# Performance work log

Hardware: AMD Instinct MI355X
Metric: run time of the kernel (lower is better)

Reference implementation:

```python
import jax, jax.numpy as jnp
import numpy as np

N, E_RAND, IN, HID, OUT = 10000, 320000, 512, 256, 256
E = E_RAND + N  # random edges + self loops
TEMP, LAM, LAMBDA_LOSS, BN_EPS = 0.5, 1e-3, 1.0, 1e-5


def _normalize(x):
    # F.normalize: x / max(||x||, 1e-12)
    return x / jnp.maximum(jnp.linalg.norm(x, axis=-1, keepdims=True), 1e-12)


def setup_inputs() -> dict:
    key = jax.random.key(0)
    ks = jax.random.split(key, 12)
    feat = jax.random.normal(ks[0], (N, IN), jnp.float32)
    loops = jnp.arange(N)
    src = jnp.concatenate([jax.random.randint(ks[1], (E_RAND,), 0, N), loops])
    dst = jnp.concatenate([jax.random.randint(ks[2], (E_RAND,), 0, N), loops])
    def lin(k, i, o):
        return jax.random.normal(k, (i, o), jnp.float32) / np.sqrt(i).astype(np.float32)
    return {
        'feat': feat,
        'W1': lin(ks[3], IN, HID), 'b1': jnp.zeros((HID,), jnp.float32),
        'W2': lin(ks[4], HID, OUT), 'b2': jnp.zeros((OUT,), jnp.float32),
        'Wt1': lin(ks[5], IN, HID), 'bt1': jnp.zeros((HID,), jnp.float32),
        'gamma': jnp.ones((HID,), jnp.float32), 'beta': jnp.zeros((HID,), jnp.float32),
        'Wt2': lin(ks[6], HID, OUT), 'bt2': jnp.zeros((OUT,), jnp.float32),
        'Wp': lin(ks[7], HID, HID), 'bp': jnp.zeros((HID,), jnp.float32),
        'src': src, 'dst': dst,
    }


def reference(feat, W1, b1, W2, b2, Wt1, bt1, gamma, beta, Wt2, bt2, Wp, bp, src, dst):
    n = feat.shape[0]
    ones = jnp.ones(src.shape, feat.dtype)
    deg_out = jax.ops.segment_sum(ones, src, num_segments=n)
    deg_in = jax.ops.segment_sum(ones, dst, num_segments=n)
    # symmetric GCN norm per edge (self-loops included so degrees >= 1)
    norm_e = jax.lax.rsqrt(deg_out)[src] * jax.lax.rsqrt(deg_in)[dst]

    def gconv(x, W, b):
        xw = x @ W  # [n, d_out]
        agg = jax.ops.segment_sum(xw[src] * norm_e[:, None], dst, num_segments=n)
        return agg + b

    # GCN encoder (2 layers, no LN)
    h = jax.nn.relu(gconv(feat, W1, b1))
    h = gconv(h, W2, b2)

    # target MLP encoder: linear -> BN(train) -> relu -> linear
    t = feat @ Wt1 + bt1
    mu = t.mean(0)
    var = t.var(0)  # biased, as BatchNorm normalization
    t = (t - mu) * jax.lax.rsqrt(var + BN_EPS) * gamma + beta
    trans = jax.nn.relu(t) @ Wt2 + bt2

    z = _normalize(h)                    # [n, d]
    q = _normalize(trans @ Wp + bp)      # projector (num_MLP=1)

    # pos_score: per-edge sum(z[u]*q[v])/temp, mean over in-edges at v
    sim_e = jnp.einsum('ed,ed->e', z[src], q[dst]) / TEMP
    pos = jax.ops.segment_sum(sim_e, dst, num_segments=n) / deg_in

    # neg_score (neg_sample=0): dense NxN similarity row-sums
    neg_sim = jnp.exp(z @ z.T / TEMP).sum(1)           # per-node
    neg_sim2 = LAM * jnp.exp(z @ q.T / TEMP).sum(1)    # per-node
    m_e = jnp.log(neg_sim[dst] + neg_sim2[src])
    neg = jax.ops.segment_sum(m_e, dst, num_segments=n) / deg_in

    loss = jnp.mean(-pos + LAMBDA_LOSS * neg)
    return loss
```

## Files before the change

kernel.cpp:

```cpp
#include <hip/hip_runtime.h>
#include <stdint.h>


#define TEMP_INV 2.0f
#define LAMC 1.0e-3f
#define SSCALE 1.6986436f

typedef __attribute__((ext_vector_type(8))) __bf16 bf16x8;
typedef __attribute__((ext_vector_type(4))) float f32x4;

__device__ __forceinline__ unsigned short f2bf(float x) {
  union { float f; unsigned int u; } v; v.f = x;
  unsigned int r = v.u + 0x7FFFu + ((v.u >> 16) & 1u);
  return (unsigned short)(r >> 16);
}

__device__ __forceinline__ void g2lds16(const void* gc, void* l) {
  void* g = const_cast<void*>(gc);
  __builtin_amdgcn_global_load_lds(
      (__attribute__((address_space(1))) void*)g,
      (__attribute__((address_space(3))) void*)l, 16, 0, 0);
}

__global__ void k_deg(const int* __restrict__ src, const int* __restrict__ dst,
                      float* deg_out, float* deg_in, int E) {
  int i = blockIdx.x * blockDim.x + threadIdx.x;
  if (i < E) {
    atomicAdd(&deg_out[src[i]], 1.0f);
    atomicAdd(&deg_in[dst[i]], 1.0f);
  }
}

__global__ void k_rdeg(const float* __restrict__ deg_out, const float* __restrict__ deg_in,
                       float* rdo, float* rdi, float* idi, int N) {
  int i = blockIdx.x * blockDim.x + threadIdx.x;
  if (i < N) {
    float o = deg_out[i], d = deg_in[i];
    rdo[i] = rsqrtf(o);
    rdi[i] = rsqrtf(d);
    idi[i] = 1.0f / d;
  }
}

__global__ void k_scan(const float* __restrict__ deg, int* __restrict__ off, int N, int E) {
  __shared__ int sm[1024];
  int tid = threadIdx.x;
  int chunk = (N + 1023) / 1024;
  int b = tid * chunk;
  int sum = 0;
  for (int j = 0; j < chunk; j++) { int i = b + j; if (i < N) sum += (int)deg[i]; }
  sm[tid] = sum;
  __syncthreads();
  for (int s = 1; s < 1024; s <<= 1) {
    int v = (tid >= s) ? sm[tid - s] : 0;
    __syncthreads();
    sm[tid] += v;
    __syncthreads();
  }
  int run = (tid == 0) ? 0 : sm[tid - 1];
  for (int j = 0; j < chunk; j++) {
    int i = b + j;
    if (i < N) { off[i] = run; run += (int)deg[i]; }
  }
  if (tid == 0) off[N] = E;
}

__global__ void k_fill(const int* __restrict__ src, const int* __restrict__ dst,
                       const int* __restrict__ off, int* cur,
                       const float* __restrict__ rdo, const float* __restrict__ rdi,
                       int* adj, float* aw, int E) {
  int e = blockIdx.x * blockDim.x + threadIdx.x;
  if (e < E) {
    int u = src[e], v = dst[e];
    int slot = off[v] + atomicAdd(&cur[v], 1);
    adj[slot] = u;
    aw[slot] = rdo[u] * rdi[v];
  }
}

template <int K, bool BIAS>
__global__ __launch_bounds__(256, 2) void k_gemm(const float* A, const float* __restrict__ W,
                                                 const float* __restrict__ bias, float* C, int M) {
  __shared__ float At[32][68];
  __shared__ float Wl[32][256];
  int tid = threadIdx.x;
  int rg = tid >> 4, cg = tid & 15;
  int r0 = rg * 4, cb = cg * 4;
  int row0 = blockIdx.x * 64;
  float acc[4][16] = {};
  for (int k0 = 0; k0 < K; k0 += 32) {
    __syncthreads();
#pragma unroll
    for (int t = 0; t < 2; t++) {
      int lin = tid + 256 * t;
      int r = lin >> 3, k4 = (lin & 7) * 4;
      int ar = row0 + r; if (ar >= M) ar = M - 1;
      float4 a4 = *(const float4*)(A + (size_t)ar * K + k0 + k4);
      At[k4 + 0][r] = a4.x; At[k4 + 1][r] = a4.y;
      At[k4 + 2][r] = a4.z; At[k4 + 3][r] = a4.w;
    }
#pragma unroll
    for (int t = 0; t < 8; t++) {
      int lin = tid + 256 * t;
      int kk = lin >> 6, c4 = (lin & 63) * 4;
      *(float4*)&Wl[kk][c4] = *(const float4*)(W + (size_t)(k0 + kk) * 256 + c4);
    }
    __syncthreads();
#pragma unroll
    for (int k = 0; k < 32; k++) {
      float4 a4 = *(const float4*)&At[k][r0];
      float av[4] = {a4.x, a4.y, a4.z, a4.w};
#pragma unroll
      for (int t = 0; t < 4; t++) {
        float4 w4 = *(const float4*)&Wl[k][64 * t + cb];
#pragma unroll
        for (int i = 0; i < 4; i++) {
          acc[i][4 * t + 0] += av[i] * w4.x;
          acc[i][4 * t + 1] += av[i] * w4.y;
          acc[i][4 * t + 2] += av[i] * w4.z;
          acc[i][4 * t + 3] += av[i] * w4.w;
        }
      }
    }
  }
#pragma unroll
  for (int i = 0; i < 4; i++) {
    int r = row0 + r0 + i;
    if (r < M) {
      float* crow = C + (size_t)r * 256;
#pragma unroll
      for (int t = 0; t < 4; t++) {
        int c = 64 * t + cb;
        float4 v = {acc[i][4 * t], acc[i][4 * t + 1], acc[i][4 * t + 2], acc[i][4 * t + 3]};
        if constexpr (BIAS) {
          float4 b4 = *(const float4*)(bias + c);
          v.x += b4.x; v.y += b4.y; v.z += b4.z; v.w += b4.w;
        }
        *(float4*)(crow + c) = v;
      }
    }
  }
}

__global__ __launch_bounds__(256, 2) void k_gemm2(const float* __restrict__ A,
                                                  const float* __restrict__ W1f,
                                                  const float* __restrict__ W2f,
                                                  const float* __restrict__ b2f,
                                                  float* __restrict__ C1, float* __restrict__ C2,
                                                  int M) {
  __shared__ float At[32][68];
  __shared__ float Wl[2][32][256];
  int tid = threadIdx.x;
  int rg = tid >> 4, cg = tid & 15;
  int r0 = rg * 4, cb = cg * 4;
  int row0 = blockIdx.x * 64;
  float acc1[4][16] = {};
  float acc2[4][16] = {};
  for (int k0 = 0; k0 < 512; k0 += 32) {
    __syncthreads();
#pragma unroll
    for (int t = 0; t < 2; t++) {
      int lin = tid + 256 * t;
      int r = lin >> 3, k4 = (lin & 7) * 4;
      int ar = row0 + r; if (ar >= M) ar = M - 1;
      float4 a4 = *(const float4*)(A + (size_t)ar * 512 + k0 + k4);
      At[k4 + 0][r] = a4.x; At[k4 + 1][r] = a4.y;
      At[k4 + 2][r] = a4.z; At[k4 + 3][r] = a4.w;
    }
#pragma unroll
    for (int t = 0; t < 8; t++) {
      int lin = tid + 256 * t;
      int kk = lin >> 6, c4 = (lin & 63) * 4;
      *(float4*)&Wl[0][kk][c4] = *(const float4*)(W1f + (size_t)(k0 + kk) * 256 + c4);
      *(float4*)&Wl[1][kk][c4] = *(const float4*)(W2f + (size_t)(k0 + kk) * 256 + c4);
    }
    __syncthreads();
#pragma unroll
    for (int k = 0; k < 32; k++) {
      float4 a4 = *(const float4*)&At[k][r0];
      float av[4] = {a4.x, a4.y, a4.z, a4.w};
#pragma unroll
      for (int t = 0; t < 4; t++) {
        float4 w4 = *(const float4*)&Wl[0][k][64 * t + cb];
        float4 u4 = *(const float4*)&Wl[1][k][64 * t + cb];
#pragma unroll
        for (int i = 0; i < 4; i++) {
          acc1[i][4 * t + 0] += av[i] * w4.x; acc1[i][4 * t + 1] += av[i] * w4.y;
          acc1[i][4 * t + 2] += av[i] * w4.z; acc1[i][4 * t + 3] += av[i] * w4.w;
          acc2[i][4 * t + 0] += av[i] * u4.x; acc2[i][4 * t + 1] += av[i] * u4.y;
          acc2[i][4 * t + 2] += av[i] * u4.z; acc2[i][4 * t + 3] += av[i] * u4.w;
        }
      }
    }
  }
#pragma unroll
  for (int i = 0; i < 4; i++) {
    int r = row0 + r0 + i;
    if (r < M) {
#pragma unroll
      for (int t = 0; t < 4; t++) {
        int c = 64 * t + cb;
        float4 v1 = {acc1[i][4 * t], acc1[i][4 * t + 1], acc1[i][4 * t + 2], acc1[i][4 * t + 3]};
        float4 v2 = {acc2[i][4 * t], acc2[i][4 * t + 1], acc2[i][4 * t + 2], acc2[i][4 * t + 3]};
        float4 b4 = *(const float4*)(b2f + c);
        v2.x += b4.x; v2.y += b4.y; v2.z += b4.z; v2.w += b4.w;
        *(float4*)(C1 + (size_t)r * 256 + c) = v1;
        *(float4*)(C2 + (size_t)r * 256 + c) = v2;
      }
    }
  }
}

__global__ void k_bnstat(const float* __restrict__ T, float* s, float* ss, int M) {
  int c = threadIdx.x;
  int r0 = blockIdx.x * 64;
  float a = 0, b = 0;
  for (int r = r0; r < r0 + 64 && r < M; r++) {
    float v = T[(size_t)r * 256 + c];
    a += v; b += v * v;
  }
  atomicAdd(&s[c], a);
  atomicAdd(&ss[c], b);
}

__global__ void k_bnrelu(float* T, const float* __restrict__ s, const float* __restrict__ ss,
                         const float* __restrict__ g, const float* __restrict__ b, int M) {
  int r = blockIdx.x, c = threadIdx.x;
  float invM = 1.0f / (float)M;
  float mu = s[c] * invM;
  float var = ss[c] * invM - mu * mu;
  float w = rsqrtf(var + 1e-5f) * g[c];
  float v = T[(size_t)r * 256 + c];
  v = (v - mu) * w + b[c];
  T[(size_t)r * 256 + c] = fmaxf(v, 0.0f);
}

template <bool UNIT, bool RELU>
__global__ __launch_bounds__(256) void k_agg(const float* __restrict__ X, const int* __restrict__ off,
                                             const int* __restrict__ adj, const float* __restrict__ w,
                                             const float* __restrict__ bias, float* __restrict__ Y, int N) {
  int wv = threadIdx.x >> 6, ln = threadIdx.x & 63;
  int v = blockIdx.x * 4 + wv;
  if (v >= N) return;
  int s0 = off[v], s1 = off[v + 1];
  const float4* X4 = (const float4*)X;
  float4 acc = {0, 0, 0, 0};
  for (int s = s0; s < s1; s++) {
    int u = adj[s];
    float wt = UNIT ? 1.0f : w[s];
    float4 x = X4[(size_t)u * 64 + ln];
    acc.x += wt * x.x; acc.y += wt * x.y; acc.z += wt * x.z; acc.w += wt * x.w;
  }
  if constexpr (!UNIT) {
    float4 b = ((const float4*)bias)[ln];
    acc.x += b.x; acc.y += b.y; acc.z += b.z; acc.w += b.w;
  }
  if constexpr (RELU) {
    acc.x = fmaxf(acc.x, 0.f); acc.y = fmaxf(acc.y, 0.f);
    acc.z = fmaxf(acc.z, 0.f); acc.w = fmaxf(acc.w, 0.f);
  }
  ((float4*)Y)[(size_t)v * 64 + ln] = acc;
}

__global__ __launch_bounds__(256) void k_norm(float* X, unsigned short* Xb, int N, int NPAD) {
  int wv = threadIdx.x >> 6, ln = threadIdx.x & 63;
  int r = blockIdx.x * 4 + wv;
  if (r >= NPAD) return;
  if (r >= N) {
    ushort4 z = {0, 0, 0, 0};
    ((ushort4*)Xb)[(size_t)r * 64 + ln] = z;
    return;
  }
  float4 x = ((const float4*)X)[(size_t)r * 64 + ln];
  float ss = x.x * x.x + x.y * x.y + x.z * x.z + x.w * x.w;
#pragma unroll
  for (int m = 1; m < 64; m <<= 1) ss += __shfl_xor(ss, m, 64);
  float sc = 1.0f / fmaxf(sqrtf(ss), 1e-12f);
  float4 xn = {x.x * sc, x.y * sc, x.z * sc, x.w * sc};
  ((float4*)X)[(size_t)r * 64 + ln] = xn;
  float bs = sc * SSCALE;
  ushort4 b;
  b.x = f2bf(x.x * bs); b.y = f2bf(x.y * bs);
  b.z = f2bf(x.z * bs); b.w = f2bf(x.w * bs);
  ((ushort4*)Xb)[(size_t)r * 64 + ln] = b;
}

__global__ __launch_bounds__(256, 2) void k_sim(const unsigned short* __restrict__ Zb,
                                                const unsigned short* __restrict__ Qb,
                                                float* __restrict__ S1, float* __restrict__ S2,
                                                int N, int JT, int JS) {
  __shared__ __align__(1024) char LB[2][32768];
  const int tid = threadIdx.x;
  const int wv = tid >> 6, ln = tid & 63;
  const int i0 = blockIdx.x * 256;
  const int wb = wv * 64;

  auto STAGE = [&](int jt, int b) {
    int j0 = jt * 32;
    char* Lb = (char*)LB[b];
#pragma unroll
    for (int it = 0; it < 8; it++) {
      int c = it * 4 + wv;
      int L = c * 1024 + ln * 16;
      int r = L >> 9;
      int o = (L & 511) ^ ((r & 7) << 4);
      const char* g = (r < 32) ? (const char*)Zb + (size_t)(j0 + r) * 512 + o
                               : (const char*)Qb + (size_t)(j0 + r - 32) * 512 + o;
      g2lds16(g, Lb + c * 1024);
    }
  };

  int jt0 = (blockIdx.y * JT) / JS;
  int jt1 = ((blockIdx.y + 1) * JT) / JS;

  STAGE(jt0, 0);

  bf16x8 af[4][8];
#pragma unroll
  for (int rf = 0; rf < 4; rf++) {
    const char* arow = (const char*)(Zb + (size_t)(i0 + wb + rf * 16 + (ln & 15)) * 256);
#pragma unroll
    for (int kk = 0; kk < 8; kk++)
      af[rf][kk] = *(const bf16x8*)(arow + kk * 64 + ((ln >> 4) << 4));
  }

  f32x4 rs[4][2] = {};

  __syncthreads();
  int cur = 0;
  for (int jt = jt0; jt < jt1; jt++) {
    if (jt + 1 < jt1) STAGE(jt + 1, cur ^ 1);
    const char* Lb = (const char*)LB[cur];
#pragma unroll
    for (int m = 0; m < 2; m++) {
      f32x4 acc[4][2] = {};
#pragma unroll
      for (int kk = 0; kk < 8; kk++) {
#pragma unroll
        for (int cf = 0; cf < 2; cf++) {
          int brow = m * 32 + cf * 16 + (ln & 15);
          int o = (kk * 64 + ((ln >> 4) << 4)) ^ ((brow & 7) << 4);
          bf16x8 bb = *(const bf16x8*)(Lb + brow * 512 + o);
#pragma unroll
          for (int rf = 0; rf < 4; rf++)
            acc[rf][cf] = __builtin_amdgcn_mfma_f32_16x16x32_bf16(af[rf][kk], bb, acc[rf][cf], 0, 0, 0);
        }
      }
#pragma unroll
      for (int rf = 0; rf < 4; rf++)
#pragma unroll
        for (int i = 0; i < 4; i++)
          rs[rf][m][i] += exp2f(acc[rf][0][i]) + exp2f(acc[rf][1][i]);
    }
    __syncthreads();
    cur ^= 1;
  }

#pragma unroll
  for (int rf = 0; rf < 4; rf++)
#pragma unroll
    for (int m = 0; m < 2; m++)
#pragma unroll
      for (int i = 0; i < 4; i++) {
        float v = rs[rf][m][i];
        v += __shfl_xor(v, 1, 64);
        v += __shfl_xor(v, 2, 64);
        v += __shfl_xor(v, 4, 64);
        v += __shfl_xor(v, 8, 64);
        if ((ln & 15) == 0) {
          int row = i0 + wb + rf * 16 + ((ln >> 4) << 2) + i;
          if (row < N) atomicAdd(((m == 0) ? S1 : S2) + row, v);
        }
      }
}

__global__ __launch_bounds__(256) void k_final(const float* __restrict__ zsum, const float* __restrict__ q,
                                               const float* __restrict__ S1, const float* __restrict__ S2,
                                               const int* __restrict__ off, const int* __restrict__ adj,
                                               const float* __restrict__ idi, float* __restrict__ out,
                                               int N, float pad) {
  int wv = threadIdx.x >> 6, ln = threadIdx.x & 63;
  int v = blockIdx.x * 4 + wv;
  if (v >= N) return;
  float4 zs = ((const float4*)zsum)[(size_t)v * 64 + ln];
  float4 qv = ((const float4*)q)[(size_t)v * 64 + ln];
  float d = zs.x * qv.x + zs.y * qv.y + zs.z * qv.z + zs.w * qv.w;
  float s1v = S1[v] - pad;
  float lg = 0.0f;
  int e0 = off[v], e1 = off[v + 1];
  for (int s = e0 + ln; s < e1; s += 64) {
    int u = adj[s];
    lg += logf(s1v + LAMC * (S2[u] - pad));
  }
#pragma unroll
  for (int m = 1; m < 64; m <<= 1) {
    d += __shfl_xor(d, m, 64);
    lg += __shfl_xor(lg, m, 64);
  }
  if (ln == 0) {
    float inv = idi[v];
    float posv = d * inv * TEMP_INV;
    float negv = lg * inv;
    atomicAdd(out, (negv - posv) * (1.0f / (float)N));
  }
}

extern "C" void kernel_launch(void* const* d_in, const int* in_sizes, int n_in,
                              void* d_out, int out_size, void* d_ws, size_t ws_size,
                              hipStream_t stream) {
  const float* feat  = (const float*)d_in[0];
  const float* W1    = (const float*)d_in[1];
  const float* b1    = (const float*)d_in[2];
  const float* W2    = (const float*)d_in[3];
  const float* b2    = (const float*)d_in[4];
  const float* Wt1   = (const float*)d_in[5];
  const float* bt1   = (const float*)d_in[6];
  const float* gamma = (const float*)d_in[7];
  const float* beta  = (const float*)d_in[8];
  const float* Wt2   = (const float*)d_in[9];
  const float* bt2   = (const float*)d_in[10];
  const float* Wp    = (const float*)d_in[11];
  const float* bp    = (const float*)d_in[12];
  const int*   src   = (const int*)d_in[13];
  const int*   dst   = (const int*)d_in[14];
  const int N = in_sizes[0] / 512;
  const int E = in_sizes[13];
  const int NTI = (N + 255) / 256, NPAD = NTI * 256, JT = NPAD / 32;
  const int JS = 25;
  const float PADF = (float)(NPAD - N);

  char* p = (char*)d_ws;
  auto alloc = [&](size_t bytes) { char* r = p; p += (bytes + 255) & ~(size_t)255; return r; };
  float* B0 = (float*)alloc((size_t)N * 256 * 4);
  float* B1 = (float*)alloc((size_t)N * 256 * 4);
  float* B2 = (float*)alloc((size_t)N * 256 * 4);
  unsigned short* zb = (unsigned short*)alloc((size_t)NPAD * 256 * 2);
  unsigned short* qb = (unsigned short*)alloc((size_t)NPAD * 256 * 2);
  int*   off = (int*)alloc((size_t)(N + 1) * 4);
  int*   adj = (int*)alloc((size_t)E * 4);
  float* aw  = (float*)alloc((size_t)E * 4);
  char*  zblk = p;
  float* deg_out = (float*)alloc((size_t)N * 4);
  float* deg_in  = (float*)alloc((size_t)N * 4);
  int*   cur     = (int*)alloc((size_t)N * 4);
  float* S1 = (float*)alloc((size_t)N * 4);
  float* S2 = (float*)alloc((size_t)N * 4);
  float* bns  = (float*)alloc(256 * 4);
  float* bnss = (float*)alloc(256 * 4);
  size_t zbytes = (size_t)(p - zblk);
  float* rdo = (float*)alloc((size_t)N * 4);
  float* rdi = (float*)alloc((size_t)N * 4);
  float* idi = (float*)alloc((size_t)N * 4);
  (void)ws_size; (void)n_in; (void)out_size;

  hipMemsetAsync(zblk, 0, zbytes, stream);
  hipMemsetAsync(d_out, 0, 4, stream);

  int gE = (E + 255) / 256, gN = (N + 255) / 256, gb = (N + 63) / 64, gw = (N + 3) / 4;
  k_deg<<<gE, 256, 0, stream>>>(src, dst, deg_out, deg_in, E);
  k_rdeg<<<gN, 256, 0, stream>>>(deg_out, deg_in, rdo, rdi, idi, N);
  k_scan<<<1, 1024, 0, stream>>>(deg_in, off, N, E);
  k_fill<<<gE, 256, 0, stream>>>(src, dst, off, cur, rdo, rdi, adj, aw, E);

  k_gemm2<<<gb, 256, 0, stream>>>(feat, W1, Wt1, bt1, B0, B1, N);
  k_bnstat<<<(N + 63) / 64, 256, 0, stream>>>(B1, bns, bnss, N);
  k_bnrelu<<<N, 256, 0, stream>>>(B1, bns, bnss, gamma, beta, N);
  k_gemm<256, true ><<<gb, 256, 0, stream>>>(B1, Wt2, bt2, B1, N);
  k_gemm<256, true ><<<gb, 256, 0, stream>>>(B1, Wp, bp, B1, N);

  k_agg<false, true ><<<gw, 256, 0, stream>>>(B0, off, adj, aw, b1, B2, N);
  k_gemm<256, false><<<gb, 256, 0, stream>>>(B2, W2, nullptr, B0, N);
  k_agg<false, false><<<gw, 256, 0, stream>>>(B0, off, adj, aw, b2, B2, N);

  int gnp = (NPAD + 3) / 4;
  k_norm<<<gnp, 256, 0, stream>>>(B2, zb, N, NPAD);
  k_norm<<<gnp, 256, 0, stream>>>(B1, qb, N, NPAD);

  dim3 gs(NTI, JS);
  k_sim<<<gs, 256, 0, stream>>>(zb, qb, S1, S2, N, JT, JS);

  k_agg<true, false><<<gw, 256, 0, stream>>>(B2, off, adj, aw, nullptr, B0, N);
  k_final<<<gw, 256, 0, stream>>>(B0, B1, S1, S2, off, adj, idi, (float*)d_out, N, PADF);
}
```

Before: 884.4 us.

## Replace LDS-tiled fp32 GEMMs with register-only kernels reading weights from cache

```diff
diff --git a/kernel.cpp b/kernel.cpp
--- a/kernel.cpp
+++ b/kernel.cpp
@@ -79,133 +79,107 @@
 }
 
 template <int K, bool BIAS>
-__global__ __launch_bounds__(256, 2) void k_gemm(const float* A, const float* __restrict__ W,
-                                                 const float* __restrict__ bias, float* C, int M) {
-  __shared__ float At[32][68];
-  __shared__ float Wl[32][256];
+__global__ __launch_bounds__(256, 4) void k_gemmG(const float* __restrict__ A,
+                                                  const float* __restrict__ W,
+                                                  const float* __restrict__ bias,
+                                                  float* __restrict__ C, int M) {
   int tid = threadIdx.x;
   int rg = tid >> 4, cg = tid & 15;
-  int r0 = rg * 4, cb = cg * 4;
-  int row0 = blockIdx.x * 64;
-  float acc[4][16] = {};
-  for (int k0 = 0; k0 < K; k0 += 32) {
-    __syncthreads();
-#pragma unroll
-    for (int t = 0; t < 2; t++) {
-      int lin = tid + 256 * t;
-      int r = lin >> 3, k4 = (lin & 7) * 4;
-      int ar = row0 + r; if (ar >= M) ar = M - 1;
-      float4 a4 = *(const float4*)(A + (size_t)ar * K + k0 + k4);
-      At[k4 + 0][r] = a4.x; At[k4 + 1][r] = a4.y;
-      At[k4 + 2][r] = a4.z; At[k4 + 3][r] = a4.w;
-    }
-#pragma unroll
-    for (int t = 0; t < 8; t++) {
-      int lin = tid + 256 * t;
-      int kk = lin >> 6, c4 = (lin & 63) * 4;
-      *(float4*)&Wl[kk][c4] = *(const float4*)(W + (size_t)(k0 + kk) * 256 + c4);
-    }
-    __syncthreads();
-#pragma unroll
-    for (int k = 0; k < 32; k++) {
-      float4 a4 = *(const float4*)&At[k][r0];
-      float av[4] = {a4.x, a4.y, a4.z, a4.w};
+  int row0 = blockIdx.x * 32 + rg * 2;
+  int c0 = cg * 16;
+  int r0 = row0 < M ? row0 : M - 1;
+  int r1 = row0 + 1 < M ? row0 + 1 : M - 1;
+  const float* Ar0 = A + (size_t)r0 * K;
+  const float* Ar1 = A + (size_t)r1 * K;
+  float acc[2][16] = {};
+  for (int k4 = 0; k4 < K; k4 += 4) {
+    float4 a0 = *(const float4*)(Ar0 + k4);
+    float4 a1 = *(const float4*)(Ar1 + k4);
+    float a0v[4] = {a0.x, a0.y, a0.z, a0.w};
+    float a1v[4] = {a1.x, a1.y, a1.z, a1.w};
+    const float* wk = W + (size_t)k4 * 256 + c0;
+#pragma unroll
+    for (int i = 0; i < 4; i++) {
 #pragma unroll
       for (int t = 0; t < 4; t++) {
-        float4 w4 = *(const float4*)&Wl[k][64 * t + cb];
-#pragma unroll
-        for (int i = 0; i < 4; i++) {
-          acc[i][4 * t + 0] += av[i] * w4.x;
-          acc[i][4 * t + 1] += av[i] * w4.y;
-          acc[i][4 * t + 2] += av[i] * w4.z;
-          acc[i][4 * t + 3] += av[i] * w4.w;
-        }
-      }
-    }
-  }
-#pragma unroll
-  for (int i = 0; i < 4; i++) {
-    int r = row0 + r0 + i;
-    if (r < M) {
-      float* crow = C + (size_t)r * 256;
+        float4 w4 = *(const float4*)(wk + i * 256 + t * 4);
+        acc[0][4 * t + 0] += a0v[i] * w4.x; acc[0][4 * t + 1] += a0v[i] * w4.y;
+        acc[0][4 * t + 2] += a0v[i] * w4.z; acc[0][4 * t + 3] += a0v[i] * w4.w;
+        acc[1][4 * t + 0] += a1v[i] * w4.x; acc[1][4 * t + 1] += a1v[i] * w4.y;
+        acc[1][4 * t + 2] += a1v[i] * w4.z; acc[1][4 * t + 3] += a1v[i] * w4.w;
+      }
+    }
+  }
+#pragma unroll
+  for (int r = 0; r < 2; r++) {
+    int rr = row0 + r;
+    if (rr < M) {
+      float* crow = C + (size_t)rr * 256 + c0;
 #pragma unroll
       for (int t = 0; t < 4; t++) {
-        int c = 64 * t + cb;
-        float4 v = {acc[i][4 * t], acc[i][4 * t + 1], acc[i][4 * t + 2], acc[i][4 * t + 3]};
+        float4 v = {acc[r][4 * t], acc[r][4 * t + 1], acc[r][4 * t + 2], acc[r][4 * t + 3]};
         if constexpr (BIAS) {
-          float4 b4 = *(const float4*)(bias + c);
+          float4 b4 = *(const float4*)(bias + c0 + 4 * t);
           v.x += b4.x; v.y += b4.y; v.z += b4.z; v.w += b4.w;
         }
-        *(float4*)(crow + c) = v;
-      }
-    }
-  }
-}
-
-__global__ __launch_bounds__(256, 2) void k_gemm2(const float* __restrict__ A,
-                                                  const float* __restrict__ W1f,
-                                                  const float* __restrict__ W2f,
-                                                  const float* __restrict__ b2f,
-                                                  float* __restrict__ C1, float* __restrict__ C2,
-                                                  int M) {
-  __shared__ float At[32][68];
-  __shared__ float Wl[2][32][256];
+        *(float4*)(crow + t * 4) = v;
+      }
+    }
+  }
+}
+
+__global__ __launch_bounds__(256, 2) void k_gemm2G(const float* __restrict__ A,
+                                                   const float* __restrict__ W1f,
+                                                   const float* __restrict__ W2f,
+                                                   const float* __restrict__ b2f,
+                                                   float* __restrict__ C1, float* __restrict__ C2,
+                                                   int M) {
   int tid = threadIdx.x;
   int rg = tid >> 4, cg = tid & 15;
-  int r0 = rg * 4, cb = cg * 4;
-  int row0 = blockIdx.x * 64;
-  float acc1[4][16] = {};
-  float acc2[4][16] = {};
-  for (int k0 = 0; k0 < 512; k0 += 32) {
-    __syncthreads();
-#pragma unroll
-    for (int t = 0; t < 2; t++) {
-      int lin = tid + 256 * t;
-      int r = lin >> 3, k4 = (lin & 7) * 4;
-      int ar = row0 + r; if (ar >= M) ar = M - 1;
-      float4 a4 = *(const float4*)(A + (size_t)ar * 512 + k0 + k4);
-      At[k4 + 0][r] = a4.x; At[k4 + 1][r] = a4.y;
-      At[k4 + 2][r] = a4.z; At[k4 + 3][r] = a4.w;
-    }
-#pragma unroll
-    for (int t = 0; t < 8; t++) {
-      int lin = tid + 256 * t;
-      int kk = lin >> 6, c4 = (lin & 63) * 4;
-      *(float4*)&Wl[0][kk][c4] = *(const float4*)(W1f + (size_t)(k0 + kk) * 256 + c4);
-      *(float4*)&Wl[1][kk][c4] = *(const float4*)(W2f + (size_t)(k0 + kk) * 256 + c4);
-    }
-    __syncthreads();
-#pragma unroll
-    for (int k = 0; k < 32; k++) {
-      float4 a4 = *(const float4*)&At[k][r0];
-      float av[4] = {a4.x, a4.y, a4.z, a4.w};
+  int row0 = blockIdx.x * 32 + rg * 2;
+  int c0 = cg * 16;
+  int r0 = row0 < M ? row0 : M - 1;
+  int r1 = row0 + 1 < M ? row0 + 1 : M - 1;
+  const float* Ar0 = A + (size_t)r0 * 512;
+  const float* Ar1 = A + (size_t)r1 * 512;
+  float acc1[2][16] = {};
+  float acc2[2][16] = {};
+  for (int k4 = 0; k4 < 512; k4 += 4) {
+    float4 a0 = *(const float4*)(Ar0 + k4);
+    float4 a1 = *(const float4*)(Ar1 + k4);
+    float a0v[4] = {a0.x, a0.y, a0.z, a0.w};
+    float a1v[4] = {a1.x, a1.y, a1.z, a1.w};
+    const float* wk1 = W1f + (size_t)k4 * 256 + c0;
+    const float* wk2 = W2f + (size_t)k4 * 256 + c0;
+#pragma unroll
+    for (int i = 0; i < 4; i++) {
 #pragma unroll
       for (int t = 0; t < 4; t++) {
-        float4 w4 = *(const float4*)&Wl[0][k][64 * t + cb];
-        float4 u4 = *(const float4*)&Wl[1][k][64 * t + cb];
-#pragma unroll
-        for (int i = 0; i < 4; i++) {
-          acc1[i][4 * t + 0] += av[i] * w4.x; acc1[i][4 * t + 1] += av[i] * w4.y;
-          acc1[i][4 * t + 2] += av[i] * w4.z; acc1[i][4 * t + 3] += av[i] * w4.w;
-          acc2[i][4 * t + 0] += av[i] * u4.x; acc2[i][4 * t + 1] += av[i] * u4.y;
-          acc2[i][4 * t + 2] += av[i] * u4.z; acc2[i][4 * t + 3] += av[i] * u4.w;
-        }
-      }
-    }
-  }
-#pragma unroll
-  for (int i = 0; i < 4; i++) {
-    int r = row0 + r0 + i;
-    if (r < M) {
+        float4 w4 = *(const float4*)(wk1 + i * 256 + t * 4);
+        float4 u4 = *(const float4*)(wk2 + i * 256 + t * 4);
+        acc1[0][4 * t + 0] += a0v[i] * w4.x; acc1[0][4 * t + 1] += a0v[i] * w4.y;
+        acc1[0][4 * t + 2] += a0v[i] * w4.z; acc1[0][4 * t + 3] += a0v[i] * w4.w;
+        acc1[1][4 * t + 0] += a1v[i] * w4.x; acc1[1][4 * t + 1] += a1v[i] * w4.y;
+        acc1[1][4 * t + 2] += a1v[i] * w4.z; acc1[1][4 * t + 3] += a1v[i] * w4.w;
+        acc2[0][4 * t + 0] += a0v[i] * u4.x; acc2[0][4 * t + 1] += a0v[i] * u4.y;
+        acc2[0][4 * t + 2] += a0v[i] * u4.z; acc2[0][4 * t + 3] += a0v[i] * u4.w;
+        acc2[1][4 * t + 0] += a1v[i] * u4.x; acc2[1][4 * t + 1] += a1v[i] * u4.y;
+        acc2[1][4 * t + 2] += a1v[i] * u4.z; acc2[1][4 * t + 3] += a1v[i] * u4.w;
+      }
+    }
+  }
+#pragma unroll
+  for (int r = 0; r < 2; r++) {
+    int rr = row0 + r;
+    if (rr < M) {
 #pragma unroll
       for (int t = 0; t < 4; t++) {
-        int c = 64 * t + cb;
-        float4 v1 = {acc1[i][4 * t], acc1[i][4 * t + 1], acc1[i][4 * t + 2], acc1[i][4 * t + 3]};
-        float4 v2 = {acc2[i][4 * t], acc2[i][4 * t + 1], acc2[i][4 * t + 2], acc2[i][4 * t + 3]};
-        float4 b4 = *(const float4*)(b2f + c);
+        float4 v1 = {acc1[r][4 * t], acc1[r][4 * t + 1], acc1[r][4 * t + 2], acc1[r][4 * t + 3]};
+        float4 v2 = {acc2[r][4 * t], acc2[r][4 * t + 1], acc2[r][4 * t + 2], acc2[r][4 * t + 3]};
+        float4 b4 = *(const float4*)(b2f + c0 + 4 * t);
         v2.x += b4.x; v2.y += b4.y; v2.z += b4.z; v2.w += b4.w;
-        *(float4*)(C1 + (size_t)r * 256 + c) = v1;
-        *(float4*)(C2 + (size_t)r * 256 + c) = v2;
+        *(float4*)(C1 + (size_t)rr * 256 + c0 + 4 * t) = v1;
+        *(float4*)(C2 + (size_t)rr * 256 + c0 + 4 * t) = v2;
       }
     }
   }
@@ -456,20 +430,20 @@
   hipMemsetAsync(zblk, 0, zbytes, stream);
   hipMemsetAsync(d_out, 0, 4, stream);
 
-  int gE = (E + 255) / 256, gN = (N + 255) / 256, gb = (N + 63) / 64, gw = (N + 3) / 4;
+  int gE = (E + 255) / 256, gN = (N + 255) / 256, gb = (N + 31) / 32, gw = (N + 3) / 4;
   k_deg<<<gE, 256, 0, stream>>>(src, dst, deg_out, deg_in, E);
   k_rdeg<<<gN, 256, 0, stream>>>(deg_out, deg_in, rdo, rdi, idi, N);
   k_scan<<<1, 1024, 0, stream>>>(deg_in, off, N, E);
   k_fill<<<gE, 256, 0, stream>>>(src, dst, off, cur, rdo, rdi, adj, aw, E);
 
-  k_gemm2<<<gb, 256, 0, stream>>>(feat, W1, Wt1, bt1, B0, B1, N);
+  k_gemm2G<<<gb, 256, 0, stream>>>(feat, W1, Wt1, bt1, B0, B1, N);
   k_bnstat<<<(N + 63) / 64, 256, 0, stream>>>(B1, bns, bnss, N);
   k_bnrelu<<<N, 256, 0, stream>>>(B1, bns, bnss, gamma, beta, N);
-  k_gemm<256, true ><<<gb, 256, 0, stream>>>(B1, Wt2, bt2, B1, N);
-  k_gemm<256, true ><<<gb, 256, 0, stream>>>(B1, Wp, bp, B1, N);
+  k_gemmG<256, true ><<<gb, 256, 0, stream>>>(B1, Wt2, bt2, B1, N);
+  k_gemmG<256, true ><<<gb, 256, 0, stream>>>(B1, Wp, bp, B1, N);
 
   k_agg<false, true ><<<gw, 256, 0, stream>>>(B0, off, adj, aw, b1, B2, N);
-  k_gemm<256, false><<<gb, 256, 0, stream>>>(B2, W2, nullptr, B0, N);
+  k_gemmG<256, false><<<gb, 256, 0, stream>>>(B2, W2, nullptr, B0, N);
   k_agg<false, false><<<gw, 256, 0, stream>>>(B0, off, adj, aw, b2, B2, N);
 
   int gnp = (NPAD + 3) / 4;
```

New measurement: 1.438 ms. +62.6%, slower.
